# Performance work log

Hardware: AMD Instinct MI355X
Metric: run time of the kernel (lower is better)

Reference implementation:

```python
import jax, jax.numpy as jnp
import numpy as np

NUM_HEADS = 16
MASK_NEG = -66504.0  # matches IPEX causal mask fill value


def setup_inputs() -> dict:
    key = jax.random.key(0)
    ks = jax.random.split(key, 5)
    B, S, E = 1, 2048, 2048
    return {
        "hidden_states": jax.random.normal(ks[0], (B, S, E), dtype=jnp.float32),
        "q_wei": jax.random.normal(ks[1], (E, E), dtype=jnp.float32) * (E ** -0.5),
        "k_wei": jax.random.normal(ks[2], (E, E), dtype=jnp.float32) * (E ** -0.5),
        "v_wei": jax.random.normal(ks[3], (E, E), dtype=jnp.float32) * (E ** -0.5),
        "out_wei": jax.random.normal(ks[4], (E, E), dtype=jnp.float32) * (E ** -0.5),
    }


def reference(hidden_states, q_wei, k_wei, v_wei, out_wei):
    B, S, E = hidden_states.shape
    H = NUM_HEADS
    D = E // H
    # qkv_normal (row-major path): x @ W, [B,S,E]
    q = hidden_states @ q_wei
    k = hidden_states @ k_wei
    v = hidden_states @ v_wei
    # compute_qkv view + normal_combine permute -> [B,H,S,D]
    q = q.reshape(B, S, H, D).transpose(0, 2, 1, 3)
    k = k.reshape(B, S, H, D).transpose(0, 2, 1, 3)
    v = v.reshape(B, S, H, D).transpose(0, 2, 1, 3)
    # naive_self_attention: scores, causal mask add, THEN scale divide
    scores = jnp.einsum("bhqd,bhkd->bhqk", q, k)  # [B,H,S,S]
    causal = jnp.triu(jnp.full((S, S), MASK_NEG, dtype=scores.dtype), k=1)
    scores = scores + causal[None, None]
    scores = scores / jnp.sqrt(jnp.asarray(D, dtype=scores.dtype))
    probs = jax.nn.softmax(scores.astype(jnp.float32), axis=-1).astype(q.dtype)
    attn = jnp.einsum("bhqk,bhkd->bhqd", probs, v)  # [B,H,S,D]
    # merge heads and output projection
    attn = attn.transpose(0, 2, 1, 3).reshape(B, S, E)
    return attn @ out_wei
```

## Files before the change

kernel.cpp:

```cpp
#include <hip/hip_runtime.h>

#define F16 _Float16
typedef __attribute__((ext_vector_type(8))) _Float16 half8;
typedef __attribute__((ext_vector_type(4))) float f32x4;

constexpr int S = 2048;
constexpr int E = 2048;
constexpr float MASK_NEG = -66504.0f;
constexpr float INV_SQRT_D = 0.08838834764831845f;
constexpr float MASK_SC = MASK_NEG * INV_SQRT_D;

__device__ __forceinline__ void gload16(const void* g, void* l) {
  __builtin_amdgcn_global_load_lds((const __attribute__((address_space(1))) void*)g,
                                   (__attribute__((address_space(3))) void*)l, 16, 0, 0);
}

__global__ __launch_bounds__(256) void cast_f32_f16_k(const float* __restrict__ x,
                                                      F16* __restrict__ y) {
  size_t i = ((size_t)blockIdx.x * 256 + threadIdx.x) * 8;
  float4 a = *(const float4*)(x + i);
  float4 b = *(const float4*)(x + i + 4);
  half8 h;
  h[0] = (F16)a.x; h[1] = (F16)a.y; h[2] = (F16)a.z; h[3] = (F16)a.w;
  h[4] = (F16)b.x; h[5] = (F16)b.y; h[6] = (F16)b.z; h[7] = (F16)b.w;
  *(half8*)(y + i) = h;
}

__global__ __launch_bounds__(256) void transpose_cast2_k(const float* __restrict__ W0,
                                                         const float* __restrict__ W1,
                                                         F16* __restrict__ D0,
                                                         F16* __restrict__ D1) {
  const float* W = blockIdx.z ? W1 : W0;
  F16* Wt = blockIdx.z ? D1 : D0;
  __shared__ float tile[64][65];
  const int t = threadIdx.x;
  const int bx = blockIdx.x, by = blockIdx.y;
  {
    int r = t >> 4, c = (t & 15) << 2;
    const float* src = W + (size_t)(by * 64 + r) * E + bx * 64 + c;
    #pragma unroll
    for (int i = 0; i < 4; ++i) {
      float4 v = *(const float4*)(src + (size_t)i * 16 * E);
      tile[r + i * 16][c + 0] = v.x; tile[r + i * 16][c + 1] = v.y;
      tile[r + i * 16][c + 2] = v.z; tile[r + i * 16][c + 3] = v.w;
    }
  }
  __syncthreads();
  {
    int r = t >> 2, c = (t & 3) << 4;
    half8 v0, v1;
    #pragma unroll
    for (int i = 0; i < 8; ++i) v0[i] = (F16)tile[c + i][r];
    #pragma unroll
    for (int i = 0; i < 8; ++i) v1[i] = (F16)tile[c + 8 + i][r];
    F16* dst = Wt + (size_t)(bx * 64 + r) * E + by * 64 + c;
    *(half8*)dst = v0;
    *(half8*)(dst + 8) = v1;
  }
}

template <int MODE>
__global__ __launch_bounds__(256, 2) void gemm_bt_k(const F16* __restrict__ A,
                                                    const F16* __restrict__ Bt,
                                                    void* __restrict__ C0v,
                                                    void* __restrict__ C1v) {
  constexpr int K = 2048, N = 2048;
  __shared__ F16 sA[128 * 64];
  __shared__ F16 sB[128 * 64];
  const int t = threadIdx.x;
  const int lane = t & 63, wave = t >> 6;
  const int wr = wave >> 1, wc = wave & 1;
  const int bm = blockIdx.y, bn = blockIdx.x;

  f32x4 acc[4][4];
  #pragma unroll
  for (int mi = 0; mi < 4; ++mi)
    #pragma unroll
    for (int ni = 0; ni < 4; ++ni) acc[mi][ni] = (f32x4){0.f, 0.f, 0.f, 0.f};

  const int rb = t >> 3;
  const int bofs = (t & 7) << 4;
  const int kOff = (bofs ^ ((rb & 7) << 4)) >> 1;
  const F16* aSrc = A + (size_t)(bm * 128 + rb) * K + kOff;
  const F16* bSrc = Bt + (size_t)(bn * 128 + rb) * K + kOff;
  F16* aDst = sA + t * 8;
  F16* bDst = sB + t * 8;

  for (int bk = 0; bk < K; bk += 64) {
    #pragma unroll
    for (int it = 0; it < 4; ++it) {
      gload16(aSrc + (size_t)it * 32 * K + bk, aDst + it * 2048);
      gload16(bSrc + (size_t)it * 32 * K + bk, bDst + it * 2048);
    }
    __syncthreads();
    #pragma unroll
    for (int kk = 0; kk < 2; ++kk) {
      half8 af[4], bf[4];
      const int kb = kk * 64 + ((lane >> 4) << 4);
      #pragma unroll
      for (int i = 0; i < 4; ++i) {
        const int ra = wr * 64 + i * 16 + (lane & 15);
        af[i] = *(const half8*)((const char*)sA + ra * 128 + (kb ^ ((ra & 7) << 4)));
        const int rn = wc * 64 + i * 16 + (lane & 15);
        bf[i] = *(const half8*)((const char*)sB + rn * 128 + (kb ^ ((rn & 7) << 4)));
      }
      #pragma unroll
      for (int mi = 0; mi < 4; ++mi)
        #pragma unroll
        for (int ni = 0; ni < 4; ++ni)
          acc[mi][ni] = __builtin_amdgcn_mfma_f32_16x16x32_f16(af[mi], bf[ni], acc[mi][ni], 0, 0, 0);
    }
    __syncthreads();
  }

  const float scale = (MODE == 1 && bn < 16) ? INV_SQRT_D : 1.0f;
  void* Cv = (MODE == 1 && bn >= 16) ? C1v : C0v;
  const int cb = (MODE == 1 ? (bn & 15) : bn) * 128;

  #pragma unroll
  for (int mi = 0; mi < 4; ++mi) {
    const int r0 = bm * 128 + wr * 64 + mi * 16 + ((lane >> 4) << 2);
    #pragma unroll
    for (int ni = 0; ni < 4; ++ni) {
      const int c = cb + wc * 64 + ni * 16 + (lane & 15);
      #pragma unroll
      for (int j = 0; j < 4; ++j) {
        if (MODE == 2)
          ((float*)Cv)[(size_t)(r0 + j) * N + c] = acc[mi][ni][j];
        else
          ((F16*)Cv)[(size_t)(r0 + j) * N + c] = (F16)(acc[mi][ni][j] * scale);
      }
    }
  }
}

__global__ __launch_bounds__(256, 2) void attn_fwd_k(const F16* __restrict__ Q,
                                                     const F16* __restrict__ Km,
                                                     const F16* __restrict__ Vt,
                                                     F16* __restrict__ O) {
  __shared__ F16 sK[2][64 * 128];
  __shared__ F16 sV[2][128 * 64];
  __shared__ F16 sP[64 * 64];
  const int t = threadIdx.x, lane = t & 63, w = t >> 6;
  const int h = blockIdx.x & 15, qt = 31 - (blockIdx.x >> 4);
  const int qrow0 = qt * 64 + w * 16;

  half8 qf[4];
  {
    const int r = qrow0 + (lane & 15);
    const F16* qp = Q + (size_t)r * E + h * 128 + ((lane >> 4) << 3);
    #pragma unroll
    for (int kd = 0; kd < 4; ++kd) qf[kd] = *(const half8*)(qp + kd * 32);
  }

  f32x4 oacc[8];
  #pragma unroll
  for (int i = 0; i < 8; ++i) oacc[i] = (f32x4){0.f, 0.f, 0.f, 0.f};
  float mrow[4] = {-3e38f, -3e38f, -3e38f, -3e38f};
  float lrow[4] = {0.f, 0.f, 0.f, 0.f};

  const int rk = t >> 4;
  const int kcol = (((t & 15) << 4) ^ ((rk & 15) << 4)) >> 1;
  const int rv = t >> 3;
  const int vcol = (((t & 7) << 4) ^ ((rv & 7) << 4)) >> 1;
  const F16* kBase = Km + (size_t)rk * E + h * 128 + kcol;
  const F16* vBase = Vt + (size_t)(h * 128 + rv) * S + vcol;

  auto stage = [&](int kt, int b) {
    const F16* kSrc = kBase + (size_t)kt * 64 * E;
    const F16* vSrc = vBase + kt * 64;
    #pragma unroll
    for (int it = 0; it < 4; ++it) {
      gload16(kSrc + (size_t)it * 16 * E, &sK[b][t * 8 + it * 2048]);
      gload16(vSrc + (size_t)it * 32 * S, &sV[b][t * 8 + it * 2048]);
    }
  };

  stage(0, 0);

  for (int kt = 0; kt <= qt; ++kt) {
    __syncthreads();
    if (kt < qt) stage(kt + 1, (kt + 1) & 1);
    const char* bK = (const char*)sK[kt & 1];
    const char* bV = (const char*)sV[kt & 1];

    f32x4 sacc[4];
    #pragma unroll
    for (int i = 0; i < 4; ++i) sacc[i] = (f32x4){0.f, 0.f, 0.f, 0.f};
    #pragma unroll
    for (int kd = 0; kd < 4; ++kd) {
      const int kb = kd * 64 + ((lane >> 4) << 4);
      #pragma unroll
      for (int ni = 0; ni < 4; ++ni) {
        const int rn = ni * 16 + (lane & 15);
        half8 bf = *(const half8*)(bK + rn * 256 + (kb ^ ((rn & 15) << 4)));
        sacc[ni] = __builtin_amdgcn_mfma_f32_16x16x32_f16(qf[kd], bf, sacc[ni], 0, 0, 0);
      }
    }

    const bool diag = (kt == qt);
    float pvv[4][4];
    const int qg0 = qrow0 + ((lane >> 4) << 2);
    const int kg0 = kt * 64 + (lane & 15);
    #pragma unroll
    for (int j = 0; j < 4; ++j) {
      float mx = -3e38f;
      #pragma unroll
      for (int ni = 0; ni < 4; ++ni) {
        float s = sacc[ni][j];
        if (diag && (kg0 + ni * 16) > (qg0 + j)) s += MASK_SC;
        pvv[ni][j] = s;
        mx = fmaxf(mx, s);
      }
      mx = fmaxf(mx, __shfl_xor(mx, 1));
      mx = fmaxf(mx, __shfl_xor(mx, 2));
      mx = fmaxf(mx, __shfl_xor(mx, 4));
      mx = fmaxf(mx, __shfl_xor(mx, 8));
      const float mnew = fmaxf(mrow[j], mx);
      const float sc = __expf(mrow[j] - mnew);
      float rs = 0.f;
      #pragma unroll
      for (int ni = 0; ni < 4; ++ni) {
        const float p = __expf(pvv[ni][j] - mnew);
        pvv[ni][j] = p;
        rs += p;
      }
      rs += __shfl_xor(rs, 1);
      rs += __shfl_xor(rs, 2);
      rs += __shfl_xor(rs, 4);
      rs += __shfl_xor(rs, 8);
      lrow[j] = lrow[j] * sc + rs;
      mrow[j] = mnew;
      #pragma unroll
      for (int df = 0; df < 8; ++df) oacc[df][j] *= sc;
    }

    {
      const int rl0 = w * 16 + ((lane >> 4) << 2);
      #pragma unroll
      for (int ni = 0; ni < 4; ++ni) {
        const int cb = (ni * 16 + (lane & 15)) * 2;
        #pragma unroll
        for (int j = 0; j < 4; ++j) {
          const int r = rl0 + j;
          *(F16*)((char*)sP + r * 128 + (cb ^ ((r & 7) << 4))) = (F16)pvv[ni][j];
        }
      }
    }

    #pragma unroll
    for (int kk = 0; kk < 2; ++kk) {
      const int kb = kk * 64 + ((lane >> 4) << 4);
      const int ra = w * 16 + (lane & 15);
      half8 pa = *(const half8*)((const char*)sP + ra * 128 + (kb ^ ((ra & 7) << 4)));
      #pragma unroll
      for (int df = 0; df < 8; ++df) {
        const int rd = df * 16 + (lane & 15);
        half8 vf = *(const half8*)(bV + rd * 128 + (kb ^ ((rd & 7) << 4)));
        oacc[df] = __builtin_amdgcn_mfma_f32_16x16x32_f16(pa, vf, oacc[df], 0, 0, 0);
      }
    }
  }

  #pragma unroll
  for (int j = 0; j < 4; ++j) {
    const float inv = 1.0f / lrow[j];
    const int r = qrow0 + ((lane >> 4) << 2) + j;
    F16* op = O + (size_t)r * E + h * 128 + (lane & 15);
    #pragma unroll
    for (int df = 0; df < 8; ++df) op[df * 16] = (F16)(oacc[df][j] * inv);
  }
}

extern "C" void kernel_launch(void* const* d_in, const int* in_sizes, int n_in,
                              void* d_out, int out_size, void* d_ws, size_t ws_size,
                              hipStream_t stream) {
  const float* X  = (const float*)d_in[0];
  const float* Wq = (const float*)d_in[1];
  const float* Wk = (const float*)d_in[2];
  const float* Wv = (const float*)d_in[3];
  const float* Wo = (const float*)d_in[4];
  float* out = (float*)d_out;

  const size_t MAT = (size_t)2048 * 2048;
  F16* Xh  = (F16*)d_ws;
  F16* Wt0 = Xh + MAT;
  F16* Wt1 = Wt0 + MAT;
  F16* Qh  = Wt1 + MAT;
  F16* Kh  = Qh + MAT;
  F16* Vh  = Kh + MAT;

  dim3 b256(256);
  cast_f32_f16_k<<<dim3(MAT / 2048), b256, 0, stream>>>(X, Xh);

  transpose_cast2_k<<<dim3(32, 32, 2), b256, 0, stream>>>(Wq, Wk, Wt0, Wt1);
  gemm_bt_k<1><<<dim3(32, 16), b256, 0, stream>>>(Xh, Wt0, Qh, Kh);

  transpose_cast2_k<<<dim3(32, 32, 2), b256, 0, stream>>>(Wv, Wo, Wt0, Wt1);
  gemm_bt_k<0><<<dim3(16, 16), b256, 0, stream>>>(Wt0, Xh, Vh, nullptr);

  attn_fwd_k<<<dim3(512), b256, 0, stream>>>(Qh, Kh, Vh, Xh);

  gemm_bt_k<2><<<dim3(16, 16), b256, 0, stream>>>(Xh, Wt1, out, nullptr);
}
```

Before: 196.2 us.

## Split attention KV range across warps and read K/V directly from global

Each attention block now handles a 32-row query tile, and its four warps form two query groups times two KV halves. Each warp reads K and V fragments straight from global memory instead of staging them in double-buffered LDS, and the two partial softmax states are merged through shared memory at the end. The grid doubles, query tiles are interleaved to balance the causal workload, launch bounds allow more blocks per CU, and setprio hints are placed around the MFMA sections. In exchange the kernel loses LDS reuse of K/V across warps and relies on cache hits for the uncoalesced fragment loads.

After: 274.9 us. 1.4x slower.

```diff
diff --git a/kernel.cpp b/kernel.cpp
--- a/kernel.cpp
+++ b/kernel.cpp
@@ -134,21 +134,30 @@
   }
 }
 
-__global__ __launch_bounds__(256, 2) void attn_fwd_k(const F16* __restrict__ Q,
+__global__ __launch_bounds__(256, 4) void attn_fwd_k(const F16* __restrict__ Q,
                                                      const F16* __restrict__ Km,
                                                      const F16* __restrict__ Vt,
                                                      F16* __restrict__ O) {
-  __shared__ F16 sK[2][64 * 128];
-  __shared__ F16 sV[2][128 * 64];
-  __shared__ F16 sP[64 * 64];
+  __shared__ float sO[2][16 * 132];
+  __shared__ float sM[2][16], sL[2][16];
+  __shared__ F16 sP[4][16 * 64];
   const int t = threadIdx.x, lane = t & 63, w = t >> 6;
-  const int h = blockIdx.x & 15, qt = 31 - (blockIdx.x >> 4);
-  const int qrow0 = qt * 64 + w * 16;
+  const int h = blockIdx.x & 15;
+  const int bq = blockIdx.x >> 4;
+  const int quarter = bq >> 4, idx = bq & 15;
+  const int qtile = (quarter == 0) ? idx
+                  : (quarter == 1) ? 63 - idx
+                  : (quarter == 2) ? 16 + idx
+                                   : 47 - idx;
+  const int qg = w & 1, split = w >> 1;
+  const int qrow0 = qtile * 32 + qg * 16;
+  const int nt = (qrow0 >> 6) + 1;
+  const int k0 = split ? (nt >> 1) : 0;
+  const int k1 = split ? nt : (nt >> 1);
 
   half8 qf[4];
   {
-    const int r = qrow0 + (lane & 15);
-    const F16* qp = Q + (size_t)r * E + h * 128 + ((lane >> 4) << 3);
+    const F16* qp = Q + (size_t)(qrow0 + (lane & 15)) * E + h * 128 + ((lane >> 4) << 3);
     #pragma unroll
     for (int kd = 0; kd < 4; ++kd) qf[kd] = *(const half8*)(qp + kd * 32);
   }
@@ -159,47 +168,26 @@
   float mrow[4] = {-3e38f, -3e38f, -3e38f, -3e38f};
   float lrow[4] = {0.f, 0.f, 0.f, 0.f};
 
-  const int rk = t >> 4;
-  const int kcol = (((t & 15) << 4) ^ ((rk & 15) << 4)) >> 1;
-  const int rv = t >> 3;
-  const int vcol = (((t & 7) << 4) ^ ((rv & 7) << 4)) >> 1;
-  const F16* kBase = Km + (size_t)rk * E + h * 128 + kcol;
-  const F16* vBase = Vt + (size_t)(h * 128 + rv) * S + vcol;
-
-  auto stage = [&](int kt, int b) {
-    const F16* kSrc = kBase + (size_t)kt * 64 * E;
-    const F16* vSrc = vBase + kt * 64;
-    #pragma unroll
-    for (int it = 0; it < 4; ++it) {
-      gload16(kSrc + (size_t)it * 16 * E, &sK[b][t * 8 + it * 2048]);
-      gload16(vSrc + (size_t)it * 32 * S, &sV[b][t * 8 + it * 2048]);
-    }
-  };
-
-  stage(0, 0);
-
-  for (int kt = 0; kt <= qt; ++kt) {
-    __syncthreads();
-    if (kt < qt) stage(kt + 1, (kt + 1) & 1);
-    const char* bK = (const char*)sK[kt & 1];
-    const char* bV = (const char*)sV[kt & 1];
-
+  const F16* kBase = Km + (size_t)(lane & 15) * E + h * 128 + ((lane >> 4) << 3);
+  const F16* vBase = Vt + ((size_t)h * 128 + (lane & 15)) * S + ((lane >> 4) << 3);
+  F16* myP = (F16*)sP[w];
+
+  for (int kt = k0; kt < k1; ++kt) {
     f32x4 sacc[4];
     #pragma unroll
     for (int i = 0; i < 4; ++i) sacc[i] = (f32x4){0.f, 0.f, 0.f, 0.f};
+    __builtin_amdgcn_s_setprio(1);
     #pragma unroll
     for (int kd = 0; kd < 4; ++kd) {
-      const int kb = kd * 64 + ((lane >> 4) << 4);
       #pragma unroll
       for (int ni = 0; ni < 4; ++ni) {
-        const int rn = ni * 16 + (lane & 15);
-        half8 bf = *(const half8*)(bK + rn * 256 + (kb ^ ((rn & 15) << 4)));
+        half8 bf = *(const half8*)(kBase + ((size_t)kt * 64 + ni * 16) * E + kd * 32);
         sacc[ni] = __builtin_amdgcn_mfma_f32_16x16x32_f16(qf[kd], bf, sacc[ni], 0, 0, 0);
       }
     }
-
-    const bool diag = (kt == qt);
-    float pvv[4][4];
+    __builtin_amdgcn_s_setprio(0);
+
+    const bool diag = (kt == nt - 1);
     const int qg0 = qrow0 + ((lane >> 4) << 2);
     const int kg0 = kt * 64 + (lane & 15);
     #pragma unroll
@@ -209,7 +197,7 @@
       for (int ni = 0; ni < 4; ++ni) {
         float s = sacc[ni][j];
         if (diag && (kg0 + ni * 16) > (qg0 + j)) s += MASK_SC;
-        pvv[ni][j] = s;
+        sacc[ni][j] = s;
         mx = fmaxf(mx, s);
       }
       mx = fmaxf(mx, __shfl_xor(mx, 1));
@@ -221,8 +209,8 @@
       float rs = 0.f;
       #pragma unroll
       for (int ni = 0; ni < 4; ++ni) {
-        const float p = __expf(pvv[ni][j] - mnew);
-        pvv[ni][j] = p;
+        const float p = __expf(sacc[ni][j] - mnew);
+        sacc[ni][j] = p;
         rs += p;
       }
       rs += __shfl_xor(rs, 1);
@@ -236,39 +224,60 @@
     }
 
     {
-      const int rl0 = w * 16 + ((lane >> 4) << 2);
+      const int rl0 = (lane >> 4) << 2;
       #pragma unroll
       for (int ni = 0; ni < 4; ++ni) {
         const int cb = (ni * 16 + (lane & 15)) * 2;
         #pragma unroll
         for (int j = 0; j < 4; ++j) {
           const int r = rl0 + j;
-          *(F16*)((char*)sP + r * 128 + (cb ^ ((r & 7) << 4))) = (F16)pvv[ni][j];
+          *(F16*)((char*)myP + r * 128 + (cb ^ ((r & 7) << 4))) = (F16)sacc[ni][j];
         }
       }
     }
 
+    __builtin_amdgcn_s_setprio(1);
     #pragma unroll
     for (int kk = 0; kk < 2; ++kk) {
       const int kb = kk * 64 + ((lane >> 4) << 4);
-      const int ra = w * 16 + (lane & 15);
-      half8 pa = *(const half8*)((const char*)sP + ra * 128 + (kb ^ ((ra & 7) << 4)));
+      const int ra = lane & 15;
+      half8 pa = *(const half8*)((const char*)myP + ra * 128 + (kb ^ ((ra & 7) << 4)));
       #pragma unroll
       for (int df = 0; df < 8; ++df) {
-        const int rd = df * 16 + (lane & 15);
-        half8 vf = *(const half8*)(bV + rd * 128 + (kb ^ ((rd & 7) << 4)));
+        half8 vf = *(const half8*)(vBase + (size_t)df * 16 * S + kt * 64 + kk * 32);
         oacc[df] = __builtin_amdgcn_mfma_f32_16x16x32_f16(pa, vf, oacc[df], 0, 0, 0);
       }
     }
-  }
-
-  #pragma unroll
-  for (int j = 0; j < 4; ++j) {
-    const float inv = 1.0f / lrow[j];
-    const int r = qrow0 + ((lane >> 4) << 2) + j;
-    F16* op = O + (size_t)r * E + h * 128 + (lane & 15);
-    #pragma unroll
-    for (int df = 0; df < 8; ++df) op[df * 16] = (F16)(oacc[df][j] * inv);
+    __builtin_amdgcn_s_setprio(0);
+  }
+
+  const int r0 = (lane >> 4) << 2;
+  if (w >= 2) {
+    float* ob = sO[w - 2];
+    #pragma unroll
+    for (int j = 0; j < 4; ++j) {
+      #pragma unroll
+      for (int df = 0; df < 8; ++df)
+        ob[(r0 + j) * 132 + df * 16 + (lane & 15)] = oacc[df][j];
+      if ((lane & 15) == 0) { sM[w - 2][r0 + j] = mrow[j]; sL[w - 2][r0 + j] = lrow[j]; }
+    }
+  }
+  __syncthreads();
+  if (w < 2) {
+    const float* ob = sO[w];
+    #pragma unroll
+    for (int j = 0; j < 4; ++j) {
+      const float m2 = sM[w][r0 + j], l2 = sL[w][r0 + j];
+      const float mn = fmaxf(mrow[j], m2);
+      const float a1 = __expf(mrow[j] - mn), a2 = __expf(m2 - mn);
+      const float inv = 1.0f / (lrow[j] * a1 + l2 * a2);
+      F16* op = O + (size_t)(qrow0 + r0 + j) * E + h * 128 + (lane & 15);
+      #pragma unroll
+      for (int df = 0; df < 8; ++df) {
+        const float v = (oacc[df][j] * a1 + ob[(r0 + j) * 132 + df * 16 + (lane & 15)] * a2) * inv;
+        op[df * 16] = (F16)v;
+      }
+    }
   }
 }
 
@@ -299,7 +308,7 @@
   transpose_cast2_k<<<dim3(32, 32, 2), b256, 0, stream>>>(Wv, Wo, Wt0, Wt1);
   gemm_bt_k<0><<<dim3(16, 16), b256, 0, stream>>>(Wt0, Xh, Vh, nullptr);
 
-  attn_fwd_k<<<dim3(512), b256, 0, stream>>>(Qh, Kh, Vh, Xh);
+  attn_fwd_k<<<dim3(1024), b256, 0, stream>>>(Qh, Kh, Vh, Xh);
 
   gemm_bt_k<2><<<dim3(16, 16), b256, 0, stream>>>(Xh, Wt1, out, nullptr);
 }
```
